# Kernel optimization log

Measured on AMD Instinct MI355X. Metric: run time of the kernel, lower is better.

Reference implementation:

```python
import jax, jax.numpy as jnp
import numpy as np


def setup_inputs() -> dict:
    key = jax.random.key(0)
    ks = jax.random.split(key, 8)
    B, T, Hh, Ww, C = 4, 1024, 64, 64, 256
    f = lambda k, s: jax.random.normal(k, s, dtype=jnp.float32)
    return {
        "query_row": f(ks[0], (B, T, C)),
        "query_col": f(ks[1], (B, T, C)),
        "key_row": f(ks[2], (B, Hh, Ww, C)),
        "key_col": f(ks[3], (B, Hh, Ww, C)),
        "value": f(ks[4], (B, Hh, Ww, C)),
        "in_proj_weight": f(ks[5], (5 * C, C)) * 0.02,
        "in_proj_bias": jnp.zeros((5 * C,), jnp.float32),
        "out_w": f(ks[6], (C, C)) * 0.02,
        "out_b": jnp.zeros((C,), jnp.float32),
        "lin_w": f(ks[7], (C, C)) * 0.02,
        "lin_b": jnp.zeros((C,), jnp.float32),
        "num_heads": 8,
    }


def reference(query_row, query_col, key_row, key_col, value,
              in_proj_weight, in_proj_bias, out_w, out_b, lin_w, lin_b,
              num_heads):
    B, T, C = query_row.shape
    Hh, Ww = key_col.shape[1], key_row.shape[2]
    nh = num_heads
    hd = C // nh
    scaling = float(hd) ** -0.5
    W5 = in_proj_weight.reshape(5, C, C)
    b5 = in_proj_bias.reshape(5, C)
    # pooled sigmoid gate over value: AdaptiveAvgPool2d(1) == mean over H,W
    v_avg = jax.nn.sigmoid(value.mean(axis=(1, 2)) @ lin_w.T + lin_b)  # [B, C]
    q_row = (query_row @ W5[0].T + b5[0]) * scaling                    # [B, T, C]
    q_col = (query_col @ W5[1].T + b5[1]) * scaling                    # [B, T, C]
    k_row = (key_row @ W5[2].T + b5[2]).mean(axis=1) * v_avg[:, None, :]  # [B, W, C]
    k_col = (key_col @ W5[3].T + b5[3]).mean(axis=2) * v_avg[:, None, :]  # [B, H, C]
    v = value @ W5[4].T + b5[4]                                        # [B, H, W, C]
    # split heads (C -> nh*hd, same layout as torch view)
    qr = q_row.reshape(B, T, nh, hd)
    qc = q_col.reshape(B, T, nh, hd)
    kr = k_row.reshape(B, Ww, nh, hd)
    kc = k_col.reshape(B, Hh, nh, hd)
    vh = v.reshape(B, Hh, Ww, nh, hd)
    attn_row = jax.nn.softmax(jnp.einsum('btnd,bwnd->bntw', qr, kr), axis=-1)  # [B,nh,T,W]
    attn_col = jax.nn.softmax(jnp.einsum('btnd,bhnd->bnth', qc, kc), axis=-1)  # [B,nh,T,H]
    # column attention over rows of v, then row attention combines
    out_col = jnp.einsum('bnth,bhwnd->bntwd', attn_col, vh)            # [B,nh,T,W,hd]
    out = jnp.einsum('bntw,bntwd->btnd', attn_row, out_col).reshape(B, T, C)
    attn_output = (out @ out_w.T + out_b).transpose(1, 0, 2)           # [T, B, C]
    # head-averaged outer-product attention map [T, B, H, W]
    grid = jnp.einsum('bntw,bnth->tbhw', attn_row, attn_col) / nh
    return attn_output, grid
```

## Files before the change

### kernel.cpp

```cpp
#include <hip/hip_runtime.h>
#include <hip/hip_bf16.h>
#include <math.h>

using bf16x8 = __attribute__((ext_vector_type(8))) short;
using f32x4  = __attribute__((ext_vector_type(4))) float;
using s16x4  = __attribute__((ext_vector_type(4))) short;

static __device__ __forceinline__ float sigmoidf_(float x){ return 1.f/(1.f+__expf(-x)); }
static __device__ __forceinline__ unsigned f2bfu(float f){
  union { float f; unsigned u; } x; x.f = f;
  return (x.u + 0x7FFFu + ((x.u>>16)&1u)) >> 16;
}
static __device__ __forceinline__ short f2bf(float f){ return (short)f2bfu(f); }
static __device__ __forceinline__ unsigned pack2bf(float lo, float hi){
  return (f2bfu(lo) & 0xFFFFu) | (f2bfu(hi) << 16);
}
static __device__ __forceinline__ float b2f_lo(unsigned u){ union{unsigned u; float f;}x; x.u = u<<16; return x.f; }
static __device__ __forceinline__ float b2f_hi(unsigned u){ union{unsigned u; float f;}x; x.u = u & 0xFFFF0000u; return x.f; }

__device__ __forceinline__ void mfma_body(short* As, short* Bs,
    const float* __restrict__ X, const float* __restrict__ Wm,
    const float* __restrict__ bias, float* __restrict__ Y,
    int bxm, int bxn, float scale, int mode){
  int tid = threadIdx.x;
  int m0 = bxm*128, n0 = bxn*128;
  int l = tid&63, wid = tid>>6, lo16 = l&15, g = l>>4;
  int wm = wid>>1, wn = wid&1;
  f32x4 acc[4][4] = {};
  int srow = tid>>1, skq = (tid&1)*32;
  size_t arow;
  int vb_ = 0, vw0 = 0;
  if (mode==4){
    vb_ = bxm>>5; vw0 = (bxm&31)*2;
    arow = (size_t)(vb_*4096 + (srow&63)*64 + vw0 + (srow>>6));
  } else arow = (size_t)(m0+srow);
  const float4* sa = (const float4*)(X + arow*256 + skq);
  const float4* sb = (const float4*)(Wm + (size_t)(n0+srow)*256 + skq);
  unsigned* da = (unsigned*)&As[srow*72 + skq];
  unsigned* db = (unsigned*)&Bs[srow*72 + skq];
  for (int k0=0;k0<4;k0++){
    __syncthreads();
    #pragma unroll
    for (int j=0;j<8;j++){
      float4 v = sa[j];
      da[2*j]   = pack2bf(v.x, v.y);
      da[2*j+1] = pack2bf(v.z, v.w);
      float4 u = sb[j];
      db[2*j]   = pack2bf(u.x, u.y);
      db[2*j+1] = pack2bf(u.z, u.w);
    }
    sa += 16; sb += 16;
    __syncthreads();
    bf16x8 af[4][2], bfr[4][2];
    #pragma unroll
    for (int mt=0;mt<4;mt++)
      #pragma unroll
      for (int c=0;c<2;c++)
        af[mt][c] = *(const bf16x8*)&As[(wm*64 + mt*16 + lo16)*72 + c*32 + g*8];
    #pragma unroll
    for (int nt=0;nt<4;nt++)
      #pragma unroll
      for (int c=0;c<2;c++)
        bfr[nt][c] = *(const bf16x8*)&Bs[(wn*64 + nt*16 + lo16)*72 + c*32 + g*8];
    #pragma unroll
    for (int mt=0;mt<4;mt++)
      #pragma unroll
      for (int nt=0;nt<4;nt++){
        acc[mt][nt] = __builtin_amdgcn_mfma_f32_16x16x32_bf16(af[mt][0], bfr[nt][0], acc[mt][nt], 0,0,0);
        acc[mt][nt] = __builtin_amdgcn_mfma_f32_16x16x32_bf16(af[mt][1], bfr[nt][1], acc[mt][nt], 0,0,0);
      }
  }
  if (mode==4){
    short* vdst = (short*)Y;
    int w = vw0 + wm;
    #pragma unroll
    for (int nt=0;nt<4;nt++){
      int col = n0 + wn*64 + nt*16 + lo16;
      float bv = bias[col];
      int n = col>>5, d = col&31;
      size_t base = (size_t)(vb_*8+n)*131072 + (size_t)w*2048 + d*64;
      #pragma unroll
      for (int mt=0;mt<4;mt++){
        int h0 = mt*16 + g*4;
        s16x4 s;
        #pragma unroll
        for (int r=0;r<4;r++) s[r] = f2bf(acc[mt][nt][r] + bv);
        *(s16x4*)(vdst + base + h0) = s;
      }
    }
  } else if (mode==3){
    #pragma unroll
    for (int nt=0;nt<4;nt++){
      int col = n0 + wn*64 + nt*16 + lo16;
      float bv = bias[col];
      #pragma unroll
      for (int mt=0;mt<4;mt++){
        int row = m0 + wm*64 + mt*16 + g*4;
        #pragma unroll
        for (int r=0;r<4;r++){
          int rr = row + r;
          Y[((size_t)((rr&1023)*4 + (rr>>10)))*256 + col] = acc[mt][nt][r] + bv;
        }
      }
    }
  } else {
    #pragma unroll
    for (int nt=0;nt<4;nt++){
      int col = n0 + wn*64 + nt*16 + lo16;
      float bv = bias[col];
      #pragma unroll
      for (int mt=0;mt<4;mt++){
        int row = m0 + wm*64 + mt*16 + g*4;
        #pragma unroll
        for (int r=0;r<4;r++){
          float y = acc[mt][nt][r] + bv;
          if (mode==0) y *= scale;
          Y[(size_t)(row+r)*256 + col] = y;
        }
      }
    }
  }
}

__global__ __launch_bounds__(256) void k_fat1(
    const float* __restrict__ value, const float* __restrict__ key_row,
    const float* __restrict__ key_col, float* __restrict__ vpart,
    float* __restrict__ krm, float* __restrict__ kcm,
    const float* __restrict__ query_row, const float* __restrict__ query_col,
    const float* __restrict__ ipw, const float* __restrict__ ipb,
    float* __restrict__ qr, float* __restrict__ qc,
    short* __restrict__ vpB, float scaling){
  __shared__ __align__(16) char smem[36864];
  int bx = blockIdx.x, c = threadIdx.x;
  if (bx < 640){
    float* red = (float*)smem;
    int cq = c & 63, rg = c >> 6;
    float4 s4 = make_float4(0.f,0.f,0.f,0.f);
    float oscale; float* outp_; size_t obase;
    if (bx < 128){
      int b = bx >> 5, chunk = bx & 31;
      const float4* p = (const float4*)(value + ((size_t)(b*4096 + chunk*128 + rg))*256) + cq;
      #pragma unroll 8
      for (int i=0;i<32;i++){
        float4 v = p[(size_t)i*256];
        s4.x+=v.x; s4.y+=v.y; s4.z+=v.z; s4.w+=v.w;
      }
      oscale = 1.f; outp_ = vpart; obase = (size_t)bx*256;
    } else if (bx < 384){
      int idx = bx - 128;
      int b = idx >> 6, w = idx & 63;
      const float4* p = (const float4*)(key_row + ((size_t)(b*4096 + w))*256) + cq;
      #pragma unroll 8
      for (int i=0;i<16;i++){
        float4 v = p[(size_t)(rg + 4*i)*4096];
        s4.x+=v.x; s4.y+=v.y; s4.z+=v.z; s4.w+=v.w;
      }
      oscale = 1.f/64.f; outp_ = krm; obase = (size_t)idx*256;
    } else {
      int idx = bx - 384;
      int b = idx >> 6, h = idx & 63;
      const float4* p = (const float4*)(key_col + ((size_t)((b*64+h)*64))*256) + cq;
      #pragma unroll 8
      for (int i=0;i<16;i++){
        float4 v = p[(size_t)(rg + 4*i)*64];
        s4.x+=v.x; s4.y+=v.y; s4.z+=v.z; s4.w+=v.w;
      }
      oscale = 1.f/64.f; outp_ = kcm; obase = (size_t)idx*256;
    }
    *(float4*)&red[rg*256 + cq*4] = s4;
    __syncthreads();
    if (c < 64){
      float4 a0 = *(float4*)&red[c*4];
      float4 a1 = *(float4*)&red[256 + c*4];
      float4 a2 = *(float4*)&red[512 + c*4];
      float4 a3 = *(float4*)&red[768 + c*4];
      float4 o = make_float4((a0.x+a1.x+a2.x+a3.x)*oscale, (a0.y+a1.y+a2.y+a3.y)*oscale,
                             (a0.z+a1.z+a2.z+a3.z)*oscale, (a0.w+a1.w+a2.w+a3.w)*oscale);
      *(float4*)&outp_[obase + c*4] = o;
    }
    return;
  }
  short* As = (short*)smem;
  short* Bs = (short*)(smem + 18432);
  if (bx < 768){
    int bxx = bx - 640;
    int zz = bxx>>6, rem = bxx&63;
    mfma_body(As, Bs, zz ? query_col : query_row, ipw + (zz?65536:0), ipb + (zz?256:0),
              zz ? qc : qr, rem&31, rem>>5, scaling, 0);
  } else {
    int bxx = bx - 768;
    mfma_body(As, Bs, value, ipw+262144, ipb+1024, (float*)vpB, bxx&127, bxx>>7, 1.f, 4);
  }
}

__global__ __launch_bounds__(256) void k_gemm_krkc(
    const float* __restrict__ krm, const float* __restrict__ kcm,
    const float* __restrict__ ipw, const float* __restrict__ ipb,
    const float* __restrict__ vpart, const float* __restrict__ lin_w,
    const float* __restrict__ lin_b,
    float* __restrict__ kr, float* __restrict__ kc){
  const float* X; const float* Wm; const float* bias; float* Y;
  if (blockIdx.z==0){ X=krm; Wm=ipw+131072; bias=ipb+512; Y=kr; }
  else              { X=kcm; Wm=ipw+196608; bias=ipb+768; Y=kc; }
  __shared__ float Ast[32*68];
  __shared__ float Bst[32*68];
  __shared__ float va[256];
  __shared__ float gsh[64];
  int tx = threadIdx.x, ty = threadIdx.y;
  int tid = ty*16 + tx;
  int b = blockIdx.x;
  int m0 = b*64, n0 = blockIdx.y*64;
  {
    float s = 0.f;
    #pragma unroll
    for (int i=0;i<32;i++) s += vpart[(size_t)(b*32+i)*256 + tid];
    va[tid] = s * (1.f/4096.f);
  }
  __syncthreads();
  {
    int j = tid>>2, kq = tid&3;
    const float* wrow = lin_w + (size_t)(n0+j)*256 + kq*64;
    const float* vap  = va + kq*64;
    float part = 0.f;
    #pragma unroll
    for (int k=0;k<64;k++) part += vap[k]*wrow[k];
    part += __shfl_xor(part, 1);
    part += __shfl_xor(part, 2);
    if (kq==0) gsh[j] = sigmoidf_(part + lin_b[n0+j]);
  }
  float acc[4][4];
  #pragma unroll
  for (int i=0;i<4;i++)
    #pragma unroll
    for (int j=0;j<4;j++) acc[i][j] = 0.f;

  for (int k0=0;k0<256;k0+=32){
    __syncthreads();
    #pragma unroll
    for (int p=0;p<2;p++){
      int pos = tid + p*256;
      int r = pos>>3, kq = pos&7;
      float4 xa = *(const float4*)&X[(size_t)(m0+r)*256 + k0 + kq*4];
      Ast[(kq*4+0)*68+r]=xa.x; Ast[(kq*4+1)*68+r]=xa.y;
      Ast[(kq*4+2)*68+r]=xa.z; Ast[(kq*4+3)*68+r]=xa.w;
      float4 wb = *(const float4*)&Wm[(size_t)(n0+r)*256 + k0 + kq*4];
      Bst[(kq*4+0)*68+r]=wb.x; Bst[(kq*4+1)*68+r]=wb.y;
      Bst[(kq*4+2)*68+r]=wb.z; Bst[(kq*4+3)*68+r]=wb.w;
    }
    __syncthreads();
    #pragma unroll
    for (int k=0;k<32;k++){
      float4 a  = *(const float4*)&Ast[k*68 + ty*4];
      float4 bv = *(const float4*)&Bst[k*68 + tx*4];
      acc[0][0]+=a.x*bv.x; acc[0][1]+=a.x*bv.y; acc[0][2]+=a.x*bv.z; acc[0][3]+=a.x*bv.w;
      acc[1][0]+=a.y*bv.x; acc[1][1]+=a.y*bv.y; acc[1][2]+=a.y*bv.z; acc[1][3]+=a.y*bv.w;
      acc[2][0]+=a.z*bv.x; acc[2][1]+=a.z*bv.y; acc[2][2]+=a.z*bv.z; acc[2][3]+=a.z*bv.w;
      acc[3][0]+=a.w*bv.x; acc[3][1]+=a.w*bv.y; acc[3][2]+=a.w*bv.z; acc[3][3]+=a.w*bv.w;
    }
  }
  float4 b4 = *(const float4*)&bias[n0 + tx*4];
  float4 g4 = *(const float4*)&gsh[tx*4];
  #pragma unroll
  for (int i=0;i<4;i++){
    int row = m0 + ty*4 + i;
    float4 y = make_float4((acc[i][0]+b4.x)*g4.x, (acc[i][1]+b4.y)*g4.y,
                           (acc[i][2]+b4.z)*g4.z, (acc[i][3]+b4.w)*g4.w);
    *(float4*)&Y[(size_t)row*256 + n0 + tx*4] = y;
  }
}

__global__ void k_attn(const float* __restrict__ qr, const float* __restrict__ kr,
                       const float* __restrict__ qc, const float* __restrict__ kc,
                       float* __restrict__ arNf, __hip_bfloat16* __restrict__ acNb){
  int lane = threadIdx.x;
  int tblk = blockIdx.x, n = blockIdx.y, z = blockIdx.z;
  int isCol = z >> 2, b = z & 3;
  const float* q  = isCol ? qc : qr;
  const float* kk = isCol ? kc : kr;
  int bn = b*8 + n;
  float4 kreg[8];
  const float4* kp = (const float4*)(kk + ((size_t)(b*64 + lane))*256 + n*32);
  #pragma unroll
  for (int i=0;i<8;i++) kreg[i] = kp[i];
  size_t qbase = ((size_t)(b*1024) + tblk*16)*256 + n*32;
  for (int i=0;i<16;i+=2){
    const float4* qp0 = (const float4*)(q + qbase + (size_t)i*256);
    const float4* qp1 = (const float4*)(q + qbase + (size_t)(i+1)*256);
    float s0 = 0.f, s1 = 0.f;
    #pragma unroll
    for (int j=0;j<8;j++){
      float4 a = qp0[j], c = qp1[j];
      s0 += a.x*kreg[j].x + a.y*kreg[j].y + a.z*kreg[j].z + a.w*kreg[j].w;
      s1 += c.x*kreg[j].x + c.y*kreg[j].y + c.z*kreg[j].z + c.w*kreg[j].w;
    }
    float e0 = __expf(s0), e1 = __expf(s1);
    float sm0 = e0, sm1 = e1;
    #pragma unroll
    for (int off=32; off; off>>=1){
      sm0 += __shfl_xor(sm0, off);
      sm1 += __shfl_xor(sm1, off);
    }
    float p0 = e0 / sm0, p1 = e1 / sm1;
    size_t off_ = ((size_t)bn*1024 + tblk*16 + i)*64 + lane;
    if (isCol){ ((short*)acNb)[off_] = f2bf(p0); ((short*)acNb)[off_ + 64] = f2bf(p1); }
    else      { arNf[off_] = p0; arNf[off_ + 64] = p1; }
  }
}

__global__ __launch_bounds__(256) void k_core3(
    const __hip_bfloat16* __restrict__ acB, const float* __restrict__ arN,
    const __hip_bfloat16* __restrict__ vpB, float* __restrict__ outp){
  __shared__ float ARs[64*36];
  __shared__ float P[4][32*34];
  int tid = threadIdx.x;
  int bn = blockIdx.x, tt = blockIdx.y;
  int b = bn>>3, n = bn&7;
  int t0 = tt*32;

  {
    int w = tid&63, tg = (tid>>6)*8;
    const float* src = arN + ((size_t)bn*1024 + t0 + tg)*64 + w;
    #pragma unroll
    for (int k=0;k<8;k++)
      ARs[w*36 + tg + k] = src[(size_t)k*64];
  }

  int l = tid&63, wid = tid>>6, lo16 = l&15, g = l>>4, g4 = g*4;
  bf16x8 af[2][2];
  {
    const short* ab = (const short*)acB + ((size_t)bn*1024 + t0 + lo16)*64 + g*8;
    #pragma unroll
    for (int ts=0; ts<2; ts++){
      af[ts][0] = *(const bf16x8*)(ab + ts*1024);
      af[ts][1] = *(const bf16x8*)(ab + ts*1024 + 32);
    }
  }
  __syncthreads();

  const short* vb = (const short*)vpB + (size_t)bn*131072 + (size_t)wid*32768 + lo16*64 + g*8;
  bf16x8 buf0[4], buf1[4];
  {
    const short* p0 = vb;
    buf0[0] = *(const bf16x8*)(p0);        buf0[1] = *(const bf16x8*)(p0 + 32);
    buf0[2] = *(const bf16x8*)(p0 + 1024); buf0[3] = *(const bf16x8*)(p0 + 1056);
    const short* p1 = vb + 2048;
    buf1[0] = *(const bf16x8*)(p1);        buf1[1] = *(const bf16x8*)(p1 + 32);
    buf1[2] = *(const bf16x8*)(p1 + 1024); buf1[3] = *(const bf16x8*)(p1 + 1056);
  }
  f32x4 o[2][2] = {};
  const f32x4 zz = {0.f,0.f,0.f,0.f};
  int wbase = wid*16;

  #pragma unroll 2
  for (int wi=0; wi<16; wi+=2){
    {
      bf16x8 c0=buf0[0], c1=buf0[1], c2=buf0[2], c3=buf0[3];
      const short* pn = vb + (size_t)((wi+2)&15)*2048;
      buf0[0] = *(const bf16x8*)(pn);        buf0[1] = *(const bf16x8*)(pn + 32);
      buf0[2] = *(const bf16x8*)(pn + 1024); buf0[3] = *(const bf16x8*)(pn + 1056);
      int wg = wbase + wi;
      #pragma unroll
      for (int ts=0; ts<2; ts++){
        f32x4 mlo = __builtin_amdgcn_mfma_f32_16x16x32_bf16(af[ts][0], c0, zz, 0,0,0);
        mlo = __builtin_amdgcn_mfma_f32_16x16x32_bf16(af[ts][1], c1, mlo, 0,0,0);
        f32x4 mhi = __builtin_amdgcn_mfma_f32_16x16x32_bf16(af[ts][0], c2, zz, 0,0,0);
        mhi = __builtin_amdgcn_mfma_f32_16x16x32_bf16(af[ts][1], c3, mhi, 0,0,0);
        f32x4 ar4 = *(const f32x4*)&ARs[wg*36 + ts*16 + g4];
        #pragma unroll
        for (int r=0;r<4;r++){ o[ts][0][r] += ar4[r]*mlo[r]; o[ts][1][r] += ar4[r]*mhi[r]; }
      }
    }
    {
      bf16x8 c0=buf1[0], c1=buf1[1], c2=buf1[2], c3=buf1[3];
      const short* pn = vb + (size_t)((wi+3)&15)*2048;
      buf1[0] = *(const bf16x8*)(pn);        buf1[1] = *(const bf16x8*)(pn + 32);
      buf1[2] = *(const bf16x8*)(pn + 1024); buf1[3] = *(const bf16x8*)(pn + 1056);
      int wg = wbase + wi + 1;
      #pragma unroll
      for (int ts=0; ts<2; ts++){
        f32x4 mlo = __builtin_amdgcn_mfma_f32_16x16x32_bf16(af[ts][0], c0, zz, 0,0,0);
        mlo = __builtin_amdgcn_mfma_f32_16x16x32_bf16(af[ts][1], c1, mlo, 0,0,0);
        f32x4 mhi = __builtin_amdgcn_mfma_f32_16x16x32_bf16(af[ts][0], c2, zz, 0,0,0);
        mhi = __builtin_amdgcn_mfma_f32_16x16x32_bf16(af[ts][1], c3, mhi, 0,0,0);
        f32x4 ar4 = *(const f32x4*)&ARs[wg*36 + ts*16 + g4];
        #pragma unroll
        for (int r=0;r<4;r++){ o[ts][0][r] += ar4[r]*mlo[r]; o[ts][1][r] += ar4[r]*mhi[r]; }
      }
    }
  }

  #pragma unroll
  for (int ts=0; ts<2; ts++)
    #pragma unroll
    for (int dh=0; dh<2; dh++)
      #pragma unroll
      for (int r=0;r<4;r++)
        P[wid][(ts*16 + g4 + r)*34 + dh*16 + lo16] = o[ts][dh][r];
  __syncthreads();

  float* obase = outp + ((size_t)b*1024 + t0)*256 + n*32;
  #pragma unroll
  for (int k=0;k<4;k++){
    int idx = k*256 + tid;
    int t = idx>>5, d = idx&31;
    float s = P[0][t*34+d] + P[1][t*34+d] + P[2][t*34+d] + P[3][t*34+d];
    obase[(size_t)t*256 + d] = s;
  }
}

__global__ __launch_bounds__(256) void k_fat2(
    const float* __restrict__ outp, const float* __restrict__ out_w,
    const float* __restrict__ out_b, float* __restrict__ out,
    const __hip_bfloat16* __restrict__ acNb, const float* __restrict__ arNf,
    float* __restrict__ gout){
  __shared__ __align__(16) char smem[36864];
  int bx = blockIdx.x;
  if (bx < 64){
    short* As = (short*)smem;
    short* Bs = (short*)(smem + 18432);
    mfma_body(As, Bs, outp, out_w, out_b, out, bx&31, bx>>5, 1.f, 3);
    return;
  }
  float* acs = (float*)smem;
  float* ars = (float*)(smem + 8192);
  int bxx = bx - 64;
  int tid = threadIdx.x, tg = bxx&255, b = bxx>>8;
  int t0 = tg*4;
  {
    int idx = tid*8;
    int n = idx>>8, t = (idx>>6)&3, x = idx&63;
    const short* asrc = (const short*)acNb + ((size_t)(b*8+n)*1024 + t0+t)*64 + x;
    uint4 av = *(const uint4*)asrc;
    float* ad = &acs[(n*4+t)*64 + x];
    ad[0]=b2f_lo(av.x); ad[1]=b2f_hi(av.x); ad[2]=b2f_lo(av.y); ad[3]=b2f_hi(av.y);
    ad[4]=b2f_lo(av.z); ad[5]=b2f_hi(av.z); ad[6]=b2f_lo(av.w); ad[7]=b2f_hi(av.w);
    const float4* rsrc = (const float4*)(arNf + ((size_t)(b*8+n)*1024 + t0+t)*64 + x);
    float4 r0 = rsrc[0], r1 = rsrc[1];
    *(float4*)&ars[(n*4+t)*64 + x]     = r0;
    *(float4*)&ars[(n*4+t)*64 + x + 4] = r1;
  }
  __syncthreads();
  int t_ = tid>>6, l = tid&63;
  int wg = l&3, hsel = l>>2;
  float acc[4][16];
  #pragma unroll
  for (int i=0;i<4;i++)
    #pragma unroll
    for (int j=0;j<16;j++) acc[i][j] = 0.f;
  #pragma unroll
  for (int n=0;n<8;n++){
    float4 a4 = *(const float4*)&acs[(n*4+t_)*64 + hsel*4];
    const float4* rb = (const float4*)&ars[(n*4+t_)*64 + wg*16];
    float4 r0 = rb[0], r1 = rb[1], r2 = rb[2], r3 = rb[3];
    float rr[16] = {r0.x,r0.y,r0.z,r0.w, r1.x,r1.y,r1.z,r1.w,
                    r2.x,r2.y,r2.z,r2.w, r3.x,r3.y,r3.z,r3.w};
    float aa[4] = {a4.x, a4.y, a4.z, a4.w};
    #pragma unroll
    for (int i=0;i<4;i++)
      #pragma unroll
      for (int j=0;j<16;j++) acc[i][j] += aa[i]*rr[j];
  }
  const float inv = 0.125f;
  float* dstbase = gout + ((size_t)(t0+t_)*4 + b)*4096;
  #pragma unroll
  for (int i=0;i<4;i++){
    float* dst = dstbase + (hsel*4+i)*64 + wg*16;
    #pragma unroll
    for (int jq=0;jq<4;jq++)
      *(float4*)&dst[jq*4] = make_float4(acc[i][jq*4]*inv, acc[i][jq*4+1]*inv,
                                         acc[i][jq*4+2]*inv, acc[i][jq*4+3]*inv);
  }
}

extern "C" void kernel_launch(void* const* d_in, const int* in_sizes, int n_in,
                              void* d_out, int out_size, void* d_ws, size_t ws_size,
                              hipStream_t stream){
  const float* query_row = (const float*)d_in[0];
  const float* query_col = (const float*)d_in[1];
  const float* key_row   = (const float*)d_in[2];
  const float* key_col   = (const float*)d_in[3];
  const float* value     = (const float*)d_in[4];
  const float* ipw       = (const float*)d_in[5];
  const float* ipb       = (const float*)d_in[6];
  const float* out_w     = (const float*)d_in[7];
  const float* out_b     = (const float*)d_in[8];
  const float* lin_w     = (const float*)d_in[9];
  const float* lin_b     = (const float*)d_in[10];
  float* out = (float*)d_out;
  float* ws  = (float*)d_ws;

  float* vpart = ws;
  float* krm   = ws + 32768;
  float* kcm   = ws + 98304;
  float* kr    = ws + 163840;
  float* kc    = ws + 229376;
  float* qr    = ws + 294912;
  float* qc    = ws + 1343488;
  __hip_bfloat16* vpB  = (__hip_bfloat16*)(ws + 2392064);
  float* arNf  = ws + 4489216;
  __hip_bfloat16* acNb = (__hip_bfloat16*)(ws + 6586368);
  float* outp  = ws + 7634944;

  const float scaling = 0.17677669529663687f;

  hipLaunchKernelGGL(k_fat1, dim3(1024), dim3(256), 0, stream,
                     value, key_row, key_col, vpart, krm, kcm,
                     query_row, query_col, ipw, ipb, qr, qc, (short*)vpB, scaling);

  hipLaunchKernelGGL(k_gemm_krkc, dim3(4,4,2), dim3(16,16), 0, stream,
                     krm, kcm, ipw, ipb, vpart, lin_w, lin_b, kr, kc);

  hipLaunchKernelGGL(k_attn, dim3(64,8,8), dim3(64), 0, stream,
                     qr, kr, qc, kc, arNf, acNb);

  hipLaunchKernelGGL(k_core3, dim3(32,32), dim3(256), 0, stream, acNb, arNf, vpB, outp);

  hipLaunchKernelGGL(k_fat2, dim3(1088), dim3(256), 0, stream,
                     outp, out_w, out_b, out, acNb, arNf, out + 1048576);
}
```

Measured before the change: 124.3 us.

## Fuse attention softmax into core kernel and store row probabilities as bf16

Removes the separate k_attn kernel. The row and column softmax probabilities are now computed inside the core attention kernel (k_core4), which keeps them in shared memory for the MFMA contraction and avoids a global round trip and a launch. Row attention probabilities are now written to global memory as bf16 instead of fp32 for the grid kernel, halving that traffic at some cost in precision of the grid output. The core kernel now does the dot products for its 32-row tile itself, which adds per-block latency before the MFMA loop.

```diff
diff --git a/kernel.cpp b/kernel.cpp
--- a/kernel.cpp
+++ b/kernel.cpp
@@ -269,73 +269,20 @@
   }
 }
 
-__global__ void k_attn(const float* __restrict__ qr, const float* __restrict__ kr,
-                       const float* __restrict__ qc, const float* __restrict__ kc,
-                       float* __restrict__ arNf, __hip_bfloat16* __restrict__ acNb){
-  int lane = threadIdx.x;
-  int tblk = blockIdx.x, n = blockIdx.y, z = blockIdx.z;
-  int isCol = z >> 2, b = z & 3;
-  const float* q  = isCol ? qc : qr;
-  const float* kk = isCol ? kc : kr;
-  int bn = b*8 + n;
-  float4 kreg[8];
-  const float4* kp = (const float4*)(kk + ((size_t)(b*64 + lane))*256 + n*32);
-  #pragma unroll
-  for (int i=0;i<8;i++) kreg[i] = kp[i];
-  size_t qbase = ((size_t)(b*1024) + tblk*16)*256 + n*32;
-  for (int i=0;i<16;i+=2){
-    const float4* qp0 = (const float4*)(q + qbase + (size_t)i*256);
-    const float4* qp1 = (const float4*)(q + qbase + (size_t)(i+1)*256);
-    float s0 = 0.f, s1 = 0.f;
-    #pragma unroll
-    for (int j=0;j<8;j++){
-      float4 a = qp0[j], c = qp1[j];
-      s0 += a.x*kreg[j].x + a.y*kreg[j].y + a.z*kreg[j].z + a.w*kreg[j].w;
-      s1 += c.x*kreg[j].x + c.y*kreg[j].y + c.z*kreg[j].z + c.w*kreg[j].w;
-    }
-    float e0 = __expf(s0), e1 = __expf(s1);
-    float sm0 = e0, sm1 = e1;
-    #pragma unroll
-    for (int off=32; off; off>>=1){
-      sm0 += __shfl_xor(sm0, off);
-      sm1 += __shfl_xor(sm1, off);
-    }
-    float p0 = e0 / sm0, p1 = e1 / sm1;
-    size_t off_ = ((size_t)bn*1024 + tblk*16 + i)*64 + lane;
-    if (isCol){ ((short*)acNb)[off_] = f2bf(p0); ((short*)acNb)[off_ + 64] = f2bf(p1); }
-    else      { arNf[off_] = p0; arNf[off_ + 64] = p1; }
-  }
-}
-
-__global__ __launch_bounds__(256) void k_core3(
-    const __hip_bfloat16* __restrict__ acB, const float* __restrict__ arN,
-    const __hip_bfloat16* __restrict__ vpB, float* __restrict__ outp){
+__global__ __launch_bounds__(256) void k_core4(
+    const float* __restrict__ qr, const float* __restrict__ qc,
+    const float* __restrict__ kr, const float* __restrict__ kc,
+    const __hip_bfloat16* __restrict__ vpB,
+    short* __restrict__ arB, short* __restrict__ acB,
+    float* __restrict__ outp){
   __shared__ float ARs[64*36];
+  __shared__ short ACb[32*72];
   __shared__ float P[4][32*34];
   int tid = threadIdx.x;
   int bn = blockIdx.x, tt = blockIdx.y;
   int b = bn>>3, n = bn&7;
   int t0 = tt*32;
-
-  {
-    int w = tid&63, tg = (tid>>6)*8;
-    const float* src = arN + ((size_t)bn*1024 + t0 + tg)*64 + w;
-    #pragma unroll
-    for (int k=0;k<8;k++)
-      ARs[w*36 + tg + k] = src[(size_t)k*64];
-  }
-
   int l = tid&63, wid = tid>>6, lo16 = l&15, g = l>>4, g4 = g*4;
-  bf16x8 af[2][2];
-  {
-    const short* ab = (const short*)acB + ((size_t)bn*1024 + t0 + lo16)*64 + g*8;
-    #pragma unroll
-    for (int ts=0; ts<2; ts++){
-      af[ts][0] = *(const bf16x8*)(ab + ts*1024);
-      af[ts][1] = *(const bf16x8*)(ab + ts*1024 + 32);
-    }
-  }
-  __syncthreads();
 
   const short* vb = (const short*)vpB + (size_t)bn*131072 + (size_t)wid*32768 + lo16*64 + g*8;
   bf16x8 buf0[4], buf1[4];
@@ -347,6 +294,79 @@
     buf1[0] = *(const bf16x8*)(p1);        buf1[1] = *(const bf16x8*)(p1 + 32);
     buf1[2] = *(const bf16x8*)(p1 + 1024); buf1[3] = *(const bf16x8*)(p1 + 1056);
   }
+
+  {
+    int w = l, tg = wid*8;
+    float4 kreg[8];
+    const float4* kp = (const float4*)(kr + ((size_t)(b*64) + w)*256 + n*32);
+    #pragma unroll
+    for (int i=0;i<8;i++) kreg[i] = kp[i];
+    const float* qbase = qr + ((size_t)(b*1024) + t0 + tg)*256 + n*32;
+    #pragma unroll
+    for (int k=0;k<8;k+=2){
+      const float4* q0 = (const float4*)(qbase + (size_t)k*256);
+      const float4* q1 = (const float4*)(qbase + (size_t)(k+1)*256);
+      float s0=0.f, s1=0.f;
+      #pragma unroll
+      for (int j=0;j<8;j++){
+        float4 a = q0[j], c = q1[j];
+        s0 += a.x*kreg[j].x + a.y*kreg[j].y + a.z*kreg[j].z + a.w*kreg[j].w;
+        s1 += c.x*kreg[j].x + c.y*kreg[j].y + c.z*kreg[j].z + c.w*kreg[j].w;
+      }
+      float e0 = __expf(s0), e1 = __expf(s1);
+      float m0 = e0, m1 = e1;
+      #pragma unroll
+      for (int off=32; off; off>>=1){
+        m0 += __shfl_xor(m0, off);
+        m1 += __shfl_xor(m1, off);
+      }
+      float p0 = e0/m0, p1 = e1/m1;
+      ARs[w*36 + tg + k]     = p0;
+      ARs[w*36 + tg + k + 1] = p1;
+      arB[((size_t)bn*1024 + t0 + tg + k)*64 + w]     = f2bf(p0);
+      arB[((size_t)bn*1024 + t0 + tg + k + 1)*64 + w] = f2bf(p1);
+    }
+  }
+
+  {
+    int t = tid>>3, j = tid&7;
+    float4 q[8];
+    const float4* qrow = (const float4*)(qc + ((size_t)(b*1024) + t0 + t)*256 + n*32);
+    #pragma unroll
+    for (int i=0;i<8;i++) q[i] = qrow[i];
+    float e[8]; float ssum = 0.f;
+    #pragma unroll
+    for (int k=0;k<8;k++){
+      const float4* kp = (const float4*)(kc + ((size_t)(b*64) + j*8 + k)*256 + n*32);
+      float s = 0.f;
+      #pragma unroll
+      for (int i=0;i<8;i++){
+        float4 kv = kp[i];
+        s += q[i].x*kv.x + q[i].y*kv.y + q[i].z*kv.z + q[i].w*kv.w;
+      }
+      e[k] = __expf(s); ssum += e[k];
+    }
+    ssum += __shfl_xor(ssum, 1);
+    ssum += __shfl_xor(ssum, 2);
+    ssum += __shfl_xor(ssum, 4);
+    float inv = 1.f/ssum;
+    int4 pk;
+    pk.x = (int)pack2bf(e[0]*inv, e[1]*inv);
+    pk.y = (int)pack2bf(e[2]*inv, e[3]*inv);
+    pk.z = (int)pack2bf(e[4]*inv, e[5]*inv);
+    pk.w = (int)pack2bf(e[6]*inv, e[7]*inv);
+    *(int4*)&ACb[t*72 + j*8] = pk;
+    *(int4*)(acB + ((size_t)bn*1024 + t0 + t)*64 + j*8) = pk;
+  }
+  __syncthreads();
+
+  bf16x8 af[2][2];
+  #pragma unroll
+  for (int ts=0; ts<2; ts++){
+    af[ts][0] = *(const bf16x8*)&ACb[(ts*16 + lo16)*72 + g*8];
+    af[ts][1] = *(const bf16x8*)&ACb[(ts*16 + lo16)*72 + 32 + g*8];
+  }
+
   f32x4 o[2][2] = {};
   const f32x4 zz = {0.f,0.f,0.f,0.f};
   int wbase = wid*16;
@@ -411,7 +431,7 @@
 __global__ __launch_bounds__(256) void k_fat2(
     const float* __restrict__ outp, const float* __restrict__ out_w,
     const float* __restrict__ out_b, float* __restrict__ out,
-    const __hip_bfloat16* __restrict__ acNb, const float* __restrict__ arNf,
+    const short* __restrict__ acB, const short* __restrict__ arB,
     float* __restrict__ gout){
   __shared__ __align__(16) char smem[36864];
   int bx = blockIdx.x;
@@ -429,15 +449,15 @@
   {
     int idx = tid*8;
     int n = idx>>8, t = (idx>>6)&3, x = idx&63;
-    const short* asrc = (const short*)acNb + ((size_t)(b*8+n)*1024 + t0+t)*64 + x;
-    uint4 av = *(const uint4*)asrc;
+    size_t soff = ((size_t)(b*8+n)*1024 + t0+t)*64 + x;
+    uint4 av = *(const uint4*)(acB + soff);
     float* ad = &acs[(n*4+t)*64 + x];
     ad[0]=b2f_lo(av.x); ad[1]=b2f_hi(av.x); ad[2]=b2f_lo(av.y); ad[3]=b2f_hi(av.y);
     ad[4]=b2f_lo(av.z); ad[5]=b2f_hi(av.z); ad[6]=b2f_lo(av.w); ad[7]=b2f_hi(av.w);
-    const float4* rsrc = (const float4*)(arNf + ((size_t)(b*8+n)*1024 + t0+t)*64 + x);
-    float4 r0 = rsrc[0], r1 = rsrc[1];
-    *(float4*)&ars[(n*4+t)*64 + x]     = r0;
-    *(float4*)&ars[(n*4+t)*64 + x + 4] = r1;
+    uint4 rv = *(const uint4*)(arB + soff);
+    float* rd = &ars[(n*4+t)*64 + x];
+    rd[0]=b2f_lo(rv.x); rd[1]=b2f_hi(rv.x); rd[2]=b2f_lo(rv.y); rd[3]=b2f_hi(rv.y);
+    rd[4]=b2f_lo(rv.z); rd[5]=b2f_hi(rv.z); rd[6]=b2f_lo(rv.w); rd[7]=b2f_hi(rv.w);
   }
   __syncthreads();
   int t_ = tid>>6, l = tid&63;
@@ -496,10 +516,10 @@
   float* kc    = ws + 229376;
   float* qr    = ws + 294912;
   float* qc    = ws + 1343488;
-  __hip_bfloat16* vpB  = (__hip_bfloat16*)(ws + 2392064);
-  float* arNf  = ws + 4489216;
-  __hip_bfloat16* acNb = (__hip_bfloat16*)(ws + 6586368);
-  float* outp  = ws + 7634944;
+  __hip_bfloat16* vpB = (__hip_bfloat16*)(ws + 2392064);
+  short* arB  = (short*)(ws + 4489216);
+  short* acB  = (short*)(ws + 5537792);
+  float* outp = ws + 6586368;
 
   const float scaling = 0.17677669529663687f;
 
@@ -510,11 +530,9 @@
   hipLaunchKernelGGL(k_gemm_krkc, dim3(4,4,2), dim3(16,16), 0, stream,
                      krm, kcm, ipw, ipb, vpart, lin_w, lin_b, kr, kc);
 
-  hipLaunchKernelGGL(k_attn, dim3(64,8,8), dim3(64), 0, stream,
-                     qr, kr, qc, kc, arNf, acNb);
-
-  hipLaunchKernelGGL(k_core3, dim3(32,32), dim3(256), 0, stream, acNb, arNf, vpB, outp);
+  hipLaunchKernelGGL(k_core4, dim3(32,32), dim3(256), 0, stream,
+                     qr, qc, kr, kc, vpB, arB, acB, outp);
 
   hipLaunchKernelGGL(k_fat2, dim3(1088), dim3(256), 0, stream,
-                     outp, out_w, out_b, out, acNb, arNf, out + 1048576);
-}
+                     outp, out_w, out_b, out, acB, arB, out + 1048576);
+}
```

Result: slower. 150.0 us (+20.7%).
